# Kernel optimization log

Hardware: AMD Instinct MI355X
Metric: run time of the kernel (lower is better)

## Reference

```python
import jax, jax.numpy as jnp
import numpy as np

B, C, H, W = 8, 1152, 32, 32
N = H * W


def _skew(t):
    # t: (B,3) -> (B,3,3) skew-symmetric
    z = jnp.zeros_like(t[:, 0])
    return jnp.stack([
        jnp.stack([z, -t[:, 2], t[:, 1]], axis=-1),
        jnp.stack([t[:, 2], z, -t[:, 0]], axis=-1),
        jnp.stack([-t[:, 1], t[:, 0], z], axis=-1),
    ], axis=1)


def _fundamental(K1, K2, R, t):
    E = _skew(t) @ R
    U, S, Vt = jnp.linalg.svd(E)
    S = S.at[:, 2].set(0.0)  # enforce rank-2 essential matrix
    E = U @ (S[:, :, None] * Vt)
    return jnp.linalg.inv(jnp.swapaxes(K2, 1, 2)) @ E @ jnp.linalg.inv(K1)


def setup_inputs() -> dict:
    key = jax.random.key(0)
    k1, k2, k3, k4, k5 = jax.random.split(key, 5)
    f_tar = jax.random.normal(k1, (B, C, H, W), dtype=jnp.float32)
    f_src = jax.random.normal(k2, (B, C, H, W), dtype=jnp.float32)
    # realistic invertible intrinsics: [[fx,0,cx],[0,fy,cy],[0,0,1]]
    def intrinsics(k):
        f = 30.0 + 2.0 * jax.random.uniform(k, (B, 2))
        Kt = jnp.zeros((B, 3, 3))
        Kt = Kt.at[:, 0, 0].set(f[:, 0]).at[:, 1, 1].set(f[:, 1])
        Kt = Kt.at[:, 0, 2].set(W / 2.0).at[:, 1, 2].set(H / 2.0).at[:, 2, 2].set(1.0)
        return Kt.astype(jnp.float32)
    K1 = intrinsics(k3)
    K2 = intrinsics(k4)
    # proper rotation via QR of a random matrix
    ka, kb = jax.random.split(k5)
    Q, Rm = jnp.linalg.qr(jax.random.normal(ka, (B, 3, 3)))
    Q = Q * jnp.sign(jnp.diagonal(Rm, axis1=1, axis2=2))[:, None, :]
    Q = Q * jnp.linalg.det(Q)[:, None, None]  # det = +1
    t = jax.random.normal(kb, (B, 3), dtype=jnp.float32)
    return {"f_tar": f_tar, "f_src": f_src, "K1": K1, "K2": K2,
            "R": Q.astype(jnp.float32), "t": t}


def reference(f_tar, f_src, K1, K2, R, t):
    f_src_flat = f_src.reshape(B, C, N)  # (B,C,N)
    # NOTE: torch code computes A = f_src^T @ f_tar but never uses it (dead code); omitted.

    # homogeneous pixel coords, indexing='ij': x=row index, y=col index
    ix, iy = jnp.meshgrid(jnp.arange(H, dtype=jnp.float32),
                          jnp.arange(W, dtype=jnp.float32), indexing='ij')
    combined = jnp.stack([ix.ravel(), iy.ravel(), jnp.ones(N, jnp.float32)], axis=0)  # (3,N)
    combined = jnp.broadcast_to(combined, (B, 3, N))

    F_mat = _fundamental(K1, K2, R, t)                       # (B,3,3)
    lines = F_mat @ combined                                 # (B,3,N)
    lines = lines / lines[:, 2:3, :]

    ones = jnp.ones((B, 1, N), jnp.float32)
    x0 = jnp.zeros((B, 1, N), jnp.float32)
    y0 = -lines[:, 2:3, :] / lines[:, 1:2, :]
    point_0 = jnp.concatenate([x0, y0, ones], axis=1)        # (B,3,N)
    x1 = jnp.full((B, 1, N), float(W), jnp.float32)
    y1 = -(lines[:, 2:3, :] + lines[:, 0:1, :] * W) / lines[:, 1:2, :]
    point_1 = jnp.concatenate([x1, y1, ones], axis=1)        # (B,3,N)

    # point-to-line distance for every (pixel i, line j) pair -> (B,N,N)
    diff = point_0 - point_1                                 # (B,3,N)
    p = combined[:, :, :, None] - point_0[:, :, None, :]     # (B,3,N,N) via broadcast
    d = diff[:, :, None, :]                                  # (B,3,1,N)
    cross = jnp.stack([
        p[:, 1] * d[:, 2] - p[:, 2] * d[:, 1],
        p[:, 2] * d[:, 0] - p[:, 0] * d[:, 2],
        p[:, 0] * d[:, 1] - p[:, 1] * d[:, 0],
    ], axis=1)                                               # (B,3,N,N)
    cross_norm = jnp.sqrt(jnp.sum(cross * cross, axis=1))    # (B,N,N)
    diff_norm = jnp.linalg.norm(diff, axis=1, keepdims=True) # (B,1,N)
    d_epi = cross_norm / diff_norm                           # (B,N,N)

    thre = 0.1
    weight_map = 1.0 - jax.nn.softmax(5.0 * (d_epi - thre), axis=-1)
    attention_map = jax.nn.softmax(weight_map, axis=1)       # softmax over dim=1, per torch code

    out = jnp.einsum('bij,bjc->bic', attention_map, jnp.swapaxes(f_src_flat, 1, 2))  # (B,N,C)
    return out.reshape(B, C, H, W)
```

## Files before the change

### kernel.cpp

```cpp
#include <hip/hip_runtime.h>
#include <hip/hip_bf16.h>
#include <math.h>

#define Bn 8
#define Cn 1152
#define Nn 1024

typedef short short8 __attribute__((ext_vector_type(8)));
typedef float f32x4 __attribute__((ext_vector_type(4)));

__device__ float g_csum_part[Bn * 32 * Nn];
__device__ unsigned short g_A[(size_t)Bn * Nn * Nn];
__device__ unsigned short g_fb[(size_t)Bn * Cn * Nn];

__device__ inline unsigned short f2bf(float x) {
    __hip_bfloat16 h = __float2bfloat16(x);
    unsigned short u;
    __builtin_memcpy(&u, &h, 2);
    return u;
}

__device__ inline void inv3(const float* M, float* o) {
    float a = M[0], b = M[1], c = M[2];
    float d = M[3], e = M[4], f = M[5];
    float g = M[6], h = M[7], i = M[8];
    float A0 = (e * i - f * h);
    float A1 = -(d * i - f * g);
    float A2 = (d * h - e * g);
    float det = a * A0 + b * A1 + c * A2;
    float inv = 1.0f / det;
    o[0] = A0 * inv;
    o[1] = -(b * i - c * h) * inv;
    o[2] = (b * f - c * e) * inv;
    o[3] = A1 * inv;
    o[4] = (a * i - c * g) * inv;
    o[5] = -(a * f - c * d) * inv;
    o[6] = A2 * inv;
    o[7] = -(a * h - b * g) * inv;
    o[8] = (a * e - b * d) * inv;
}

__device__ inline void mm3(const float* X, const float* Y, float* Z) {
    for (int r = 0; r < 3; r++)
        for (int c = 0; c < 3; c++)
            Z[r * 3 + c] = X[r * 3 + 0] * Y[0 * 3 + c] + X[r * 3 + 1] * Y[1 * 3 + c] +
                           X[r * 3 + 2] * Y[2 * 3 + c];
}

__device__ inline void computeF(const float* K1, const float* K2, const float* R,
                                const float* t, int b, float* F) {
    float t0 = t[b * 3 + 0], t1 = t[b * 3 + 1], t2 = t[b * 3 + 2];
    float S[9] = {0.0f, -t2, t1, t2, 0.0f, -t0, -t1, t0, 0.0f};
    float E[9];
    mm3(S, &R[b * 9], E);
    float iK1[9], iK2[9];
    inv3(&K1[b * 9], iK1);
    inv3(&K2[b * 9], iK2);
    float iK2T[9] = {iK2[0], iK2[3], iK2[6], iK2[1], iK2[4], iK2[7], iK2[2], iK2[5], iK2[8]};
    float T[9];
    mm3(iK2T, E, T);
    mm3(T, iK1, F);
}

__device__ inline float4 zcoef(const float* F, int j) {
    float jx = (float)(j >> 5);
    float jy = (float)(j & 31);
    float l0 = F[0] * jx + F[1] * jy + F[2];
    float l1 = F[3] * jx + F[4] * jy + F[5];
    float l2 = F[6] * jx + F[7] * jy + F[8];
    l0 = l0 / l2;
    l1 = l1 / l2;
    float y0 = -1.0f / l1;
    float y1 = -(1.0f + l0 * 32.0f) / l1;
    float dy = y0 - y1;
    float invn = 1.0f / sqrtf(1024.0f + dy * dy);
    return make_float4(5.0f * dy * invn, 160.0f * invn, 160.0f * y0 * invn, 0.0f);
}

__launch_bounds__(256) __global__ void fusedE_kernel(const float* __restrict__ K1,
                                                     const float* __restrict__ K2,
                                                     const float* __restrict__ R,
                                                     const float* __restrict__ t) {
    __shared__ float Fs[9];
    __shared__ float4 prm[Nn];
    __shared__ float red[4][16][64];
    int lin = blockIdx.x;
    int b = lin & 7;
    int seg = lin >> 3;
    if (threadIdx.x == 0) computeF(K1, K2, R, t, b, Fs);
    __syncthreads();
#pragma unroll
    for (int u = 0; u < 4; u++) {
        int j = threadIdx.x * 4 + u;
        prm[j] = zcoef(Fs, j);
    }
    __syncthreads();
    int wv = threadIdx.x >> 6;
    int lane = threadIdx.x & 63;
    float px[16], py[16], pz[16];
#pragma unroll
    for (int k = 0; k < 16; k++) {
        float4 p = prm[lane + k * 64];
        px[k] = p.x;
        py[k] = p.y;
        pz[k] = p.z;
    }
    float csum[16];
#pragma unroll
    for (int k = 0; k < 16; k++) csum[k] = 0.0f;
#pragma unroll
    for (int rr = 0; rr < 8; rr++) {
        int i = seg * 32 + wv * 8 + rr;
        float ix = (float)(i >> 5), iy = (float)(i & 31);
        float e[16], m = -INFINITY;
#pragma unroll
        for (int k = 0; k < 16; k++) {
            e[k] = fabsf(fmaf(ix, px[k], fmaf(iy, py[k], -pz[k]))) - 0.5f;
            m = fmaxf(m, e[k]);
        }
#pragma unroll
        for (int o = 32; o > 0; o >>= 1) m = fmaxf(m, __shfl_xor(m, o, 64));
        float s = 0.0f;
#pragma unroll
        for (int k = 0; k < 16; k++) {
            e[k] = __expf(e[k] - m);
            s += e[k];
        }
#pragma unroll
        for (int o = 32; o > 0; o >>= 1) s += __shfl_xor(s, o, 64);
        float rsi = 1.0f / s;
        unsigned short* arow = g_A + (size_t)(b * Nn + i) * Nn;
#pragma unroll
        for (int k = 0; k < 16; k++) {
            float E = __expf(1.0f - e[k] * rsi);
            csum[k] += E;
            arow[lane + k * 64] = f2bf(E);
        }
    }
#pragma unroll
    for (int k = 0; k < 16; k++) red[wv][k][lane] = csum[k];
    __syncthreads();
    int l2 = threadIdx.x & 63;
    int k0 = (threadIdx.x >> 6) * 4;
#pragma unroll
    for (int q = 0; q < 4; q++) {
        int k = k0 + q;
        float ssum = red[0][k][l2] + red[1][k][l2] + red[2][k][l2] + red[3][k][l2];
        g_csum_part[(b * 32 + seg) * Nn + k * 64 + l2] = ssum;
    }
}

__global__ void convert_fsrc_kernel(const float* __restrict__ f) {
    int lin = blockIdx.x;
    int b = lin & 7;
    int cg = lin >> 3;
    int j0 = threadIdx.x * 4;
    float4 cs = *(const float4*)&g_csum_part[(b * 32 + 0) * Nn + j0];
#pragma unroll
    for (int it = 1; it < 32; it++) {
        float4 p = *(const float4*)&g_csum_part[(b * 32 + it) * Nn + j0];
        cs.x += p.x; cs.y += p.y; cs.z += p.z; cs.w += p.w;
    }
    float4 inv = make_float4(1.0f / cs.x, 1.0f / cs.y, 1.0f / cs.z, 1.0f / cs.w);
#pragma unroll
    for (int c8 = 0; c8 < 8; c8++) {
        int c = cg * 8 + c8;
        size_t off = ((size_t)b * Cn + c) * Nn + j0;
        float4 v = *(const float4*)(f + off);
        ushort4 u;
        u.x = f2bf(v.x * inv.x);
        u.y = f2bf(v.y * inv.y);
        u.z = f2bf(v.z * inv.z);
        u.w = f2bf(v.w * inv.w);
        *(ushort4*)&g_fb[off] = u;
    }
}

#define BM 128
#define BNc 128
#define BK 32

__launch_bounds__(256, 2) __global__ void gemm_kernel(float* __restrict__ out) {
    __shared__ unsigned short As[2][BM * BK];
    __shared__ unsigned short Bs[2][BNc * BK];
    int lin = blockIdx.x;
    int b = lin & 7;
    int s = lin >> 3;
    int it = s & 7;
    int ct = s >> 3;
    int i0 = it * BM;
    int c0 = ct * BNc;
    int t = threadIdx.x;
    int w = t >> 6, L = t & 63;
    int wr = w >> 1, wc = w & 1;
    const unsigned short* Ab = g_A + (size_t)b * Nn * Nn + (size_t)i0 * Nn;
    const unsigned short* Fb = g_fb + (size_t)b * Cn * Nn + (size_t)c0 * Nn;

    auto stage = [&](int p, int kt) {
#pragma unroll
        for (int h = 0; h < 2; h++) {
            int chunk = h * 256 + t;
            int rr = chunk >> 2;
            int gq = (chunk & 3) ^ ((rr >> 1) & 3);
            const unsigned short* ga = Ab + (size_t)rr * Nn + kt + gq * 8;
            __builtin_amdgcn_global_load_lds(
                (const __attribute__((address_space(1))) unsigned int*)ga,
                (__attribute__((address_space(3))) unsigned int*)(As[p] + chunk * 8), 16, 0, 0);
            const unsigned short* gb = Fb + (size_t)rr * Nn + kt + gq * 8;
            __builtin_amdgcn_global_load_lds(
                (const __attribute__((address_space(1))) unsigned int*)gb,
                (__attribute__((address_space(3))) unsigned int*)(Bs[p] + chunk * 8), 16, 0, 0);
        }
    };

    f32x4 acc[4][4] = {};
    int lrow = L & 15, quad = L >> 4;
    stage(0, 0);
    for (int kt = 0; kt < Nn; kt += BK) {
        int p = (kt >> 5) & 1;
        __syncthreads();
        if (kt + BK < Nn) stage(1 - p, kt + BK);
        short8 af[4], bf[4];
#pragma unroll
        for (int mt = 0; mt < 4; mt++) {
            int rr = wr * 64 + mt * 16 + lrow;
            int q = quad ^ ((rr >> 1) & 3);
            af[mt] = *(const short8*)(As[p] + rr * BK + q * 8);
        }
#pragma unroll
        for (int nt = 0; nt < 4; nt++) {
            int cc = wc * 64 + nt * 16 + lrow;
            int q = quad ^ ((cc >> 1) & 3);
            bf[nt] = *(const short8*)(Bs[p] + cc * BK + q * 8);
        }
#pragma unroll
        for (int mt = 0; mt < 4; mt++)
#pragma unroll
            for (int nt = 0; nt < 4; nt++)
                acc[mt][nt] =
                    __builtin_amdgcn_mfma_f32_16x16x32_bf16(af[mt], bf[nt], acc[mt][nt], 0, 0, 0);
    }
    int col = L & 15;
#pragma unroll
    for (int mt = 0; mt < 4; mt++)
#pragma unroll
        for (int rg = 0; rg < 4; rg++) {
            int i = i0 + wr * 64 + mt * 16 + quad * 4 + rg;
            float* orow = out + ((size_t)b * Nn + i) * Cn + c0 + wc * 64;
#pragma unroll
            for (int nt = 0; nt < 4; nt++) orow[nt * 16 + col] = acc[mt][nt][rg];
        }
}

extern "C" void kernel_launch(void* const* d_in, const int* in_sizes, int n_in,
                              void* d_out, int out_size, void* d_ws, size_t ws_size,
                              hipStream_t stream) {
    (void)in_sizes; (void)n_in; (void)d_ws; (void)ws_size; (void)out_size;
    const float* f_src = (const float*)d_in[1];
    const float* K1 = (const float*)d_in[2];
    const float* K2 = (const float*)d_in[3];
    const float* R = (const float*)d_in[4];
    const float* t = (const float*)d_in[5];
    float* out = (float*)d_out;

    fusedE_kernel<<<dim3(256), dim3(256), 0, stream>>>(K1, K2, R, t);
    convert_fsrc_kernel<<<dim3(Bn * Cn / 8), dim3(256), 0, stream>>>(f_src);
    gemm_kernel<<<dim3(Bn * (Nn / BM) * (Cn / BNc)), dim3(256), 0, stream>>>(out);
}
```

Baseline: 166.6 us.

## Fuse f_src scaling and bf16 conversion into GEMM B-tile staging

Removes the separate kernel that scaled f_src by inverse column sums and wrote a bf16 copy. A tiny kernel now computes only the inverse column sums, and the GEMM loads fp32 f_src directly, scales it, converts to bf16 in registers and stores it to LDS. The N tile shrinks to 64 and launch bounds rise to 4 blocks per CU. This avoids writing and re-reading a ~19MB intermediate, but B loads become synchronous register loads instead of async global_load_lds, and each f_src element is re-read and reconverted by every row tile.

```diff
diff --git a/kernel.cpp b/kernel.cpp
--- a/kernel.cpp
+++ b/kernel.cpp
@@ -10,8 +10,8 @@
 typedef float f32x4 __attribute__((ext_vector_type(4)));
 
 __device__ float g_csum_part[Bn * 32 * Nn];
+__device__ float g_icsum[Bn * Nn];
 __device__ unsigned short g_A[(size_t)Bn * Nn * Nn];
-__device__ unsigned short g_fb[(size_t)Bn * Cn * Nn];
 
 __device__ inline unsigned short f2bf(float x) {
     __hip_bfloat16 h = __float2bfloat16(x);
@@ -150,10 +150,8 @@
     }
 }
 
-__global__ void convert_fsrc_kernel(const float* __restrict__ f) {
-    int lin = blockIdx.x;
-    int b = lin & 7;
-    int cg = lin >> 3;
+__global__ void icsum_kernel() {
+    int b = blockIdx.x;
     int j0 = threadIdx.x * 4;
     float4 cs = *(const float4*)&g_csum_part[(b * 32 + 0) * Nn + j0];
 #pragma unroll
@@ -162,27 +160,18 @@
         cs.x += p.x; cs.y += p.y; cs.z += p.z; cs.w += p.w;
     }
     float4 inv = make_float4(1.0f / cs.x, 1.0f / cs.y, 1.0f / cs.z, 1.0f / cs.w);
-#pragma unroll
-    for (int c8 = 0; c8 < 8; c8++) {
-        int c = cg * 8 + c8;
-        size_t off = ((size_t)b * Cn + c) * Nn + j0;
-        float4 v = *(const float4*)(f + off);
-        ushort4 u;
-        u.x = f2bf(v.x * inv.x);
-        u.y = f2bf(v.y * inv.y);
-        u.z = f2bf(v.z * inv.z);
-        u.w = f2bf(v.w * inv.w);
-        *(ushort4*)&g_fb[off] = u;
-    }
+    *(float4*)&g_icsum[b * Nn + j0] = inv;
 }
 
 #define BM 128
-#define BNc 128
+#define BNc 64
 #define BK 32
 
-__launch_bounds__(256, 2) __global__ void gemm_kernel(float* __restrict__ out) {
+__launch_bounds__(256, 4) __global__ void gemm_kernel(const float* __restrict__ fsrc,
+                                                      float* __restrict__ out) {
     __shared__ unsigned short As[2][BM * BK];
     __shared__ unsigned short Bs[2][BNc * BK];
+    __shared__ float ics[Nn];
     int lin = blockIdx.x;
     int b = lin & 7;
     int s = lin >> 3;
@@ -194,7 +183,13 @@
     int w = t >> 6, L = t & 63;
     int wr = w >> 1, wc = w & 1;
     const unsigned short* Ab = g_A + (size_t)b * Nn * Nn + (size_t)i0 * Nn;
-    const unsigned short* Fb = g_fb + (size_t)b * Cn * Nn + (size_t)c0 * Nn;
+    const float* Fb = fsrc + ((size_t)b * Cn + c0) * Nn;
+
+#pragma unroll
+    for (int u = 0; u < 4; u++) {
+        int j = t + u * 256;
+        ics[j] = g_icsum[b * Nn + j];
+    }
 
     auto stage = [&](int p, int kt) {
 #pragma unroll
@@ -206,21 +201,38 @@
             __builtin_amdgcn_global_load_lds(
                 (const __attribute__((address_space(1))) unsigned int*)ga,
                 (__attribute__((address_space(3))) unsigned int*)(As[p] + chunk * 8), 16, 0, 0);
-            const unsigned short* gb = Fb + (size_t)rr * Nn + kt + gq * 8;
-            __builtin_amdgcn_global_load_lds(
-                (const __attribute__((address_space(1))) unsigned int*)gb,
-                (__attribute__((address_space(3))) unsigned int*)(Bs[p] + chunk * 8), 16, 0, 0);
+        }
+        {
+            int chunk = t;
+            int rr = chunk >> 2;
+            int gq = (chunk & 3) ^ ((rr >> 1) & 3);
+            const float* gb = Fb + (size_t)rr * Nn + kt + gq * 8;
+            float4 v0 = *(const float4*)gb;
+            float4 v1 = *(const float4*)(gb + 4);
+            const float* icp = &ics[kt + gq * 8];
+            ushort4 u0, u1;
+            u0.x = f2bf(v0.x * icp[0]);
+            u0.y = f2bf(v0.y * icp[1]);
+            u0.z = f2bf(v0.z * icp[2]);
+            u0.w = f2bf(v0.w * icp[3]);
+            u1.x = f2bf(v1.x * icp[4]);
+            u1.y = f2bf(v1.y * icp[5]);
+            u1.z = f2bf(v1.z * icp[6]);
+            u1.w = f2bf(v1.w * icp[7]);
+            *(ushort4*)(Bs[p] + chunk * 8) = u0;
+            *(ushort4*)(Bs[p] + chunk * 8 + 4) = u1;
         }
     };
 
-    f32x4 acc[4][4] = {};
+    f32x4 acc[4][2] = {};
     int lrow = L & 15, quad = L >> 4;
+    __syncthreads();
     stage(0, 0);
     for (int kt = 0; kt < Nn; kt += BK) {
         int p = (kt >> 5) & 1;
         __syncthreads();
         if (kt + BK < Nn) stage(1 - p, kt + BK);
-        short8 af[4], bf[4];
+        short8 af[4], bf[2];
 #pragma unroll
         for (int mt = 0; mt < 4; mt++) {
             int rr = wr * 64 + mt * 16 + lrow;
@@ -228,15 +240,15 @@
             af[mt] = *(const short8*)(As[p] + rr * BK + q * 8);
         }
 #pragma unroll
-        for (int nt = 0; nt < 4; nt++) {
-            int cc = wc * 64 + nt * 16 + lrow;
+        for (int nt = 0; nt < 2; nt++) {
+            int cc = wc * 32 + nt * 16 + lrow;
             int q = quad ^ ((cc >> 1) & 3);
             bf[nt] = *(const short8*)(Bs[p] + cc * BK + q * 8);
         }
 #pragma unroll
         for (int mt = 0; mt < 4; mt++)
 #pragma unroll
-            for (int nt = 0; nt < 4; nt++)
+            for (int nt = 0; nt < 2; nt++)
                 acc[mt][nt] =
                     __builtin_amdgcn_mfma_f32_16x16x32_bf16(af[mt], bf[nt], acc[mt][nt], 0, 0, 0);
     }
@@ -246,9 +258,9 @@
 #pragma unroll
         for (int rg = 0; rg < 4; rg++) {
             int i = i0 + wr * 64 + mt * 16 + quad * 4 + rg;
-            float* orow = out + ((size_t)b * Nn + i) * Cn + c0 + wc * 64;
-#pragma unroll
-            for (int nt = 0; nt < 4; nt++) orow[nt * 16 + col] = acc[mt][nt][rg];
+            float* orow = out + ((size_t)b * Nn + i) * Cn + c0 + wc * 32;
+#pragma unroll
+            for (int nt = 0; nt < 2; nt++) orow[nt * 16 + col] = acc[mt][nt][rg];
         }
 }
 
@@ -264,6 +276,6 @@
     float* out = (float*)d_out;
 
     fusedE_kernel<<<dim3(256), dim3(256), 0, stream>>>(K1, K2, R, t);
-    convert_fsrc_kernel<<<dim3(Bn * Cn / 8), dim3(256), 0, stream>>>(f_src);
-    gemm_kernel<<<dim3(Bn * (Nn / BM) * (Cn / BNc)), dim3(256), 0, stream>>>(out);
-}
+    icsum_kernel<<<dim3(8), dim3(256), 0, stream>>>();
+    gemm_kernel<<<dim3(Bn * (Nn / BM) * (Cn / BNc)), dim3(256), 0, stream>>>(f_src, out);
+}
```

After: 185.1 us. +11.1%, slower.

## Load GEMM MFMA operands directly from global memory, dropping LDS staging

Applied to the files above, without the earlier changes.

The GEMM kernel no longer stages A and B tiles through double-buffered LDS with global_load_lds and barriers. Each wave now reads its MFMA operand fragments straight from global memory as 16-byte vector loads, with the k-loop unrolled by two. This removes LDS traffic, the __syncthreads barriers and the swizzle arithmetic. In exchange, operand data shared between waves is no longer reused through LDS, so L2 traffic rises, the 32-element strided row reads are less coalesced, and latency is hidden only by occupancy and unrolling.

```diff
diff --git a/kernel.cpp b/kernel.cpp
--- a/kernel.cpp
+++ b/kernel.cpp
@@ -176,63 +176,33 @@
     }
 }
 
-#define BM 128
-#define BNc 128
-#define BK 32
-
-__launch_bounds__(256, 2) __global__ void gemm_kernel(float* __restrict__ out) {
-    __shared__ unsigned short As[2][BM * BK];
-    __shared__ unsigned short Bs[2][BNc * BK];
+__launch_bounds__(256) __global__ void gemm_kernel(float* __restrict__ out) {
     int lin = blockIdx.x;
     int b = lin & 7;
     int s = lin >> 3;
     int it = s & 7;
     int ct = s >> 3;
-    int i0 = it * BM;
-    int c0 = ct * BNc;
     int t = threadIdx.x;
     int w = t >> 6, L = t & 63;
     int wr = w >> 1, wc = w & 1;
-    const unsigned short* Ab = g_A + (size_t)b * Nn * Nn + (size_t)i0 * Nn;
-    const unsigned short* Fb = g_fb + (size_t)b * Cn * Nn + (size_t)c0 * Nn;
-
-    auto stage = [&](int p, int kt) {
-#pragma unroll
-        for (int h = 0; h < 2; h++) {
-            int chunk = h * 256 + t;
-            int rr = chunk >> 2;
-            int gq = (chunk & 3) ^ ((rr >> 1) & 3);
-            const unsigned short* ga = Ab + (size_t)rr * Nn + kt + gq * 8;
-            __builtin_amdgcn_global_load_lds(
-                (const __attribute__((address_space(1))) unsigned int*)ga,
-                (__attribute__((address_space(3))) unsigned int*)(As[p] + chunk * 8), 16, 0, 0);
-            const unsigned short* gb = Fb + (size_t)rr * Nn + kt + gq * 8;
-            __builtin_amdgcn_global_load_lds(
-                (const __attribute__((address_space(1))) unsigned int*)gb,
-                (__attribute__((address_space(3))) unsigned int*)(Bs[p] + chunk * 8), 16, 0, 0);
-        }
-    };
+    int i0 = it * 128 + wr * 64;
+    int c0 = ct * 128 + wc * 64;
+    int r = L & 15, q = L >> 4;
+    const unsigned short* Ap =
+        g_A + (size_t)b * Nn * Nn + (size_t)(i0 + r) * Nn + q * 8;
+    const unsigned short* Bp =
+        g_fb + (size_t)b * Cn * Nn + (size_t)(c0 + r) * Nn + q * 8;
 
     f32x4 acc[4][4] = {};
-    int lrow = L & 15, quad = L >> 4;
-    stage(0, 0);
-    for (int kt = 0; kt < Nn; kt += BK) {
-        int p = (kt >> 5) & 1;
-        __syncthreads();
-        if (kt + BK < Nn) stage(1 - p, kt + BK);
+#pragma unroll 2
+    for (int kt = 0; kt < Nn; kt += 32) {
         short8 af[4], bf[4];
 #pragma unroll
-        for (int mt = 0; mt < 4; mt++) {
-            int rr = wr * 64 + mt * 16 + lrow;
-            int q = quad ^ ((rr >> 1) & 3);
-            af[mt] = *(const short8*)(As[p] + rr * BK + q * 8);
-        }
-#pragma unroll
-        for (int nt = 0; nt < 4; nt++) {
-            int cc = wc * 64 + nt * 16 + lrow;
-            int q = quad ^ ((cc >> 1) & 3);
-            bf[nt] = *(const short8*)(Bs[p] + cc * BK + q * 8);
-        }
+        for (int mt = 0; mt < 4; mt++)
+            af[mt] = *(const short8*)(Ap + (size_t)mt * 16 * Nn + kt);
+#pragma unroll
+        for (int nt = 0; nt < 4; nt++)
+            bf[nt] = *(const short8*)(Bp + (size_t)nt * 16 * Nn + kt);
 #pragma unroll
         for (int mt = 0; mt < 4; mt++)
 #pragma unroll
@@ -240,13 +210,13 @@
                 acc[mt][nt] =
                     __builtin_amdgcn_mfma_f32_16x16x32_bf16(af[mt], bf[nt], acc[mt][nt], 0, 0, 0);
     }
-    int col = L & 15;
+    int col = L & 15, quad = L >> 4;
 #pragma unroll
     for (int mt = 0; mt < 4; mt++)
 #pragma unroll
         for (int rg = 0; rg < 4; rg++) {
-            int i = i0 + wr * 64 + mt * 16 + quad * 4 + rg;
-            float* orow = out + ((size_t)b * Nn + i) * Cn + c0 + wc * 64;
+            int i = i0 + mt * 16 + quad * 4 + rg;
+            float* orow = out + ((size_t)b * Nn + i) * Cn + c0;
 #pragma unroll
             for (int nt = 0; nt < 4; nt++) orow[nt * 16 + col] = acc[mt][nt][rg];
         }
@@ -265,5 +235,5 @@
 
     fusedE_kernel<<<dim3(256), dim3(256), 0, stream>>>(K1, K2, R, t);
     convert_fsrc_kernel<<<dim3(Bn * Cn / 8), dim3(256), 0, stream>>>(f_src);
-    gemm_kernel<<<dim3(Bn * (Nn / BM) * (Cn / BNc)), dim3(256), 0, stream>>>(out);
-}
+    gemm_kernel<<<dim3(576), dim3(256), 0, stream>>>(out);
+}
```

Result: slower. 218.9 us (+31.4%).

## Use 4-stage LDS pipeline with 128x64 tiles and explicit vmcnt waits

Applied to the files above, without the earlier changes.

The GEMM tile shrinks from 128x128 with 4 waves to 128x64 with 2 waves, doubling the block count. The double buffer becomes a 4-deep ring with three stages in flight. Each step waits only on the oldest stage through explicit s_waitcnt vmcnt plus s_barrier, hiding more global-to-LDS latency behind the MFMA work. The cost is more LDS per block, A tiles loaded twice as often across blocks, and hand-counted vmcnt values that must match the number of loads issued per stage.

```diff
diff --git a/kernel.cpp b/kernel.cpp
--- a/kernel.cpp
+++ b/kernel.cpp
@@ -177,12 +177,13 @@
 }
 
 #define BM 128
-#define BNc 128
+#define BNc 64
 #define BK 32
-
-__launch_bounds__(256, 2) __global__ void gemm_kernel(float* __restrict__ out) {
-    __shared__ unsigned short As[2][BM * BK];
-    __shared__ unsigned short Bs[2][BNc * BK];
+#define NSTEP (Nn / BK)
+
+__launch_bounds__(128) __global__ void gemm_kernel(float* __restrict__ out) {
+    __shared__ unsigned short As[4][BM * BK];
+    __shared__ unsigned short Bs[4][BNc * BK];
     int lin = blockIdx.x;
     int b = lin & 7;
     int s = lin >> 3;
@@ -192,20 +193,25 @@
     int c0 = ct * BNc;
     int t = threadIdx.x;
     int w = t >> 6, L = t & 63;
-    int wr = w >> 1, wc = w & 1;
     const unsigned short* Ab = g_A + (size_t)b * Nn * Nn + (size_t)i0 * Nn;
     const unsigned short* Fb = g_fb + (size_t)b * Cn * Nn + (size_t)c0 * Nn;
 
     auto stage = [&](int p, int kt) {
 #pragma unroll
-        for (int h = 0; h < 2; h++) {
-            int chunk = h * 256 + t;
+        for (int h = 0; h < 4; h++) {
+            int chunk = h * 128 + t;
             int rr = chunk >> 2;
             int gq = (chunk & 3) ^ ((rr >> 1) & 3);
             const unsigned short* ga = Ab + (size_t)rr * Nn + kt + gq * 8;
             __builtin_amdgcn_global_load_lds(
                 (const __attribute__((address_space(1))) unsigned int*)ga,
                 (__attribute__((address_space(3))) unsigned int*)(As[p] + chunk * 8), 16, 0, 0);
+        }
+#pragma unroll
+        for (int h = 0; h < 2; h++) {
+            int chunk = h * 128 + t;
+            int rr = chunk >> 2;
+            int gq = (chunk & 3) ^ ((rr >> 1) & 3);
             const unsigned short* gb = Fb + (size_t)rr * Nn + kt + gq * 8;
             __builtin_amdgcn_global_load_lds(
                 (const __attribute__((address_space(1))) unsigned int*)gb,
@@ -216,20 +222,28 @@
     f32x4 acc[4][4] = {};
     int lrow = L & 15, quad = L >> 4;
     stage(0, 0);
-    for (int kt = 0; kt < Nn; kt += BK) {
-        int p = (kt >> 5) & 1;
-        __syncthreads();
-        if (kt + BK < Nn) stage(1 - p, kt + BK);
+    stage(1, BK);
+    stage(2, 2 * BK);
+    for (int st = 0; st < NSTEP; ++st) {
+        if (st < NSTEP - 2) {
+            asm volatile("s_waitcnt vmcnt(12)\n\ts_barrier" ::: "memory");
+        } else if (st == NSTEP - 2) {
+            asm volatile("s_waitcnt vmcnt(6)\n\ts_barrier" ::: "memory");
+        } else {
+            asm volatile("s_waitcnt vmcnt(0)\n\ts_barrier" ::: "memory");
+        }
+        if (st + 3 < NSTEP) stage((st + 3) & 3, (st + 3) * BK);
+        int p = st & 3;
         short8 af[4], bf[4];
 #pragma unroll
         for (int mt = 0; mt < 4; mt++) {
-            int rr = wr * 64 + mt * 16 + lrow;
+            int rr = w * 64 + mt * 16 + lrow;
             int q = quad ^ ((rr >> 1) & 3);
             af[mt] = *(const short8*)(As[p] + rr * BK + q * 8);
         }
 #pragma unroll
         for (int nt = 0; nt < 4; nt++) {
-            int cc = wc * 64 + nt * 16 + lrow;
+            int cc = nt * 16 + lrow;
             int q = quad ^ ((cc >> 1) & 3);
             bf[nt] = *(const short8*)(Bs[p] + cc * BK + q * 8);
         }
@@ -245,8 +259,8 @@
     for (int mt = 0; mt < 4; mt++)
 #pragma unroll
         for (int rg = 0; rg < 4; rg++) {
-            int i = i0 + wr * 64 + mt * 16 + quad * 4 + rg;
-            float* orow = out + ((size_t)b * Nn + i) * Cn + c0 + wc * 64;
+            int i = i0 + w * 64 + mt * 16 + quad * 4 + rg;
+            float* orow = out + ((size_t)b * Nn + i) * Cn + c0;
 #pragma unroll
             for (int nt = 0; nt < 4; nt++) orow[nt * 16 + col] = acc[mt][nt][rg];
         }
@@ -265,5 +279,5 @@
 
     fusedE_kernel<<<dim3(256), dim3(256), 0, stream>>>(K1, K2, R, t);
     convert_fsrc_kernel<<<dim3(Bn * Cn / 8), dim3(256), 0, stream>>>(f_src);
-    gemm_kernel<<<dim3(Bn * (Nn / BM) * (Cn / BNc)), dim3(256), 0, stream>>>(out);
-}
+    gemm_kernel<<<dim3(Bn * (Nn / BM) * (Cn / BNc)), dim3(128), 0, stream>>>(out);
+}
```

Result: slower. 181.9 us (+9.2%).
